# Optimization experiments

Hardware: AMD Instinct MI355X
Metric: run time of the kernel (lower is better)

## Reference

```python
import jax, jax.numpy as jnp
import numpy as np

B, N, F, T = 8, 4096, 3, 12
D = 64            # model_dim
AH, DK, DV = 4, 32, 32   # attention headers, k_dim, v_dim
GH = 8            # gat_headers == out_features
E = 524288


def _ln(x, g, b, eps=1e-5):
    m = jnp.mean(x, -1, keepdims=True)
    v = jnp.mean((x - m) ** 2, -1, keepdims=True)
    return (x - m) * jax.lax.rsqrt(v + eps) * g + b


def _glu(x, w, b, C):
    # x: [B, C, N, L], w: [2C, C, 1, k] -> causal-style valid conv + SiLU gate
    y = jax.lax.conv_general_dilated(x, w, (1, 1), 'VALID',
                                     dimension_numbers=('NCHW', 'OIHW', 'NCHW'))
    y = y + b[None, :, None, None]
    return jax.nn.silu(y[:, :C]) * y[:, C:]


def setup_inputs():
    key = jax.random.key(0)
    ks = jax.random.split(key, 20)
    s = jnp.float32(0.02)
    return {
        'data': jax.random.normal(ks[0], (B, N, F, T), jnp.float32),
        'edges': jax.random.randint(ks[1], (2, E), 0, B * N),
        'embT_w': jax.random.normal(ks[2], (T, N)) * s,
        'embT_g': jnp.ones((N,)), 'embT_b': jnp.zeros((N,)),
        'wq': jax.random.normal(ks[3], (N, AH * DK)) * s,
        'wk': jax.random.normal(ks[4], (N, AH * DK)) * s,
        'wv': jax.random.normal(ks[5], (N, AH * DV)) * s,
        'wo': jax.random.normal(ks[6], (AH * DV, N)) * s,
        'tat_g': jnp.ones((N,)), 'tat_b': jnp.zeros((N,)),
        'mix_w': jax.random.normal(ks[7], (D, T, F)) * s,
        'mix_b': jnp.zeros((D,)),
        'embS_w': jax.random.normal(ks[8], (N, D)) * s,
        'embS_g': jnp.ones((D,)), 'embS_b': jnp.zeros((D,)),
        'gat_wl': jax.random.normal(ks[9], (D, GH * T)) * s,
        'gat_bl': jnp.zeros((GH * T,)),
        'gat_wr': jax.random.normal(ks[10], (D, GH * T)) * s,
        'gat_br': jnp.zeros((GH * T,)),
        'gat_att': jax.random.normal(ks[11], (GH, T)) * s,
        'gat_bias': jnp.zeros((GH * T,)),
        'g3_w': jax.random.normal(ks[12], (2 * GH, GH, 1, 3)) * s, 'g3_b': jnp.zeros((2 * GH,)),
        'g5_w': jax.random.normal(ks[13], (2 * GH, GH, 1, 5)) * s, 'g5_b': jnp.zeros((2 * GH,)),
        'g7_w': jax.random.normal(ks[14], (2 * GH, GH, 1, 7)) * s, 'g7_b': jnp.zeros((2 * GH,)),
        'fc_w': jax.random.normal(ks[15], (3 * T - 12, T)) * s, 'fc_b': jnp.zeros((T,)),
        'res_w': jax.random.normal(ks[16], (GH, F)) * s, 'res_b': jnp.zeros((GH,)),
        'ln_g': jnp.ones((GH,)), 'ln_b': jnp.zeros((GH,)),
    }


def reference(data, edges, embT_w, embT_g, embT_b, wq, wk, wv, wo, tat_g, tat_b,
              mix_w, mix_b, embS_w, embS_g, embS_b,
              gat_wl, gat_bl, gat_wr, gat_br, gat_att, gat_bias,
              g3_w, g3_b, g5_w, g5_b, g7_w, g7_b, fc_w, fc_b,
              res_w, res_b, ln_g, ln_b):
    # ---- EmbedT: [B,N,F,T] -> [B,F,T,N] plus learned temporal positional table
    x = data.transpose(0, 2, 3, 1) + embT_w[None, None]
    x = _ln(x, embT_g, embT_b)

    # ---- Temporal MHA over T (model_dim = N), dropout = identity in eval
    resid = x
    q = (x @ wq).reshape(B, F, T, AH, DK)
    k = (x @ wk).reshape(B, F, T, AH, DK)
    v = (x @ wv).reshape(B, F, T, AH, DV)
    scores = jnp.einsum('bfqhd,bfkhd->bfhqk', q, k) / jnp.sqrt(jnp.float32(DK))
    attn = jax.nn.softmax(scores, axis=-1)
    ctx = jnp.einsum('bfhqk,bfkhd->bfqhd', attn, v).reshape(B, F, T, AH * DV)
    x = _ln(ctx @ wo + resid, tat_g, tat_b)

    # ---- feature_temporal_mixer: Conv2d(T, D, (1, F)) on [B,T,N,F] -> [B,N,D]
    x = jnp.einsum('bftn,dtf->bnd', x, mix_w) + mix_b

    # ---- EmbedS
    x = _ln(x + embS_w[None], embS_g, embS_b)

    # ---- GATv2Conv over B*N nodes (add_self_loops=True, leaky slope 0.2)
    BN = B * N
    xf = x.reshape(BN, D)
    xl = (xf @ gat_wl + gat_bl).reshape(BN, GH, T)
    xr = (xf @ gat_wr + gat_br).reshape(BN, GH, T)
    loop = jnp.arange(BN)
    src = jnp.concatenate([edges[0], loop])
    dst = jnp.concatenate([edges[1], loop])
    feat = jax.nn.leaky_relu(xl[src] + xr[dst], 0.2)          # [E+BN, GH, T]
    e = jnp.einsum('eht,ht->eh', feat, gat_att)
    m = jax.ops.segment_max(e, dst, num_segments=BN)
    ex = jnp.exp(e - m[dst])
    ssum = jax.ops.segment_sum(ex, dst, num_segments=BN)
    alpha = ex / ssum[dst]
    out = jax.ops.segment_sum(xl[src] * alpha[:, :, None], dst, num_segments=BN)
    out = out.reshape(BN, GH * T) + gat_bias

    res_gate = out.reshape(B, N, GH, T).transpose(0, 2, 1, 3)  # [B,GH,N,T]

    # ---- gated convs (GLU) kernels 3/5/7 -> concat -> fc
    g = jnp.concatenate([_glu(res_gate, g3_w, g3_b, GH),
                         _glu(res_gate, g5_w, g5_b, GH),
                         _glu(res_gate, g7_w, g7_b, GH)], axis=-1)  # [B,GH,N,3T-12]
    x = jax.nn.relu(g @ fc_w + fc_b)   # features_num == 3 branch

    # ---- residual 1x1 conv over feature channels of raw data
    x_res = jnp.einsum('bfnt,of->bont', data.transpose(0, 2, 1, 3), res_w) \
            + res_b[None, :, None, None]
    x = jax.nn.relu(x_res + x)         # [B,GH,N,T]
    x = _ln(x.transpose(0, 3, 2, 1), ln_g, ln_b)  # LN over GH on [B,T,N,GH]
    return x.transpose(0, 2, 3, 1)     # [B,N,GH,T]
```

## Files before the change

### kernel.cpp

```cpp
#include <hip/hip_runtime.h>
#include <hip/hip_bf16.h>

typedef __hip_bfloat16 bf16;
typedef short bf16x8 __attribute__((ext_vector_type(8)));
typedef float f32x4 __attribute__((ext_vector_type(4)));
typedef unsigned short u16x4 __attribute__((ext_vector_type(4)));

constexpr int B = 8, N = 4096, F = 3, T = 12;
constexpr int Dm = 64, AH = 4, DK = 32;
constexpr int GH = 8;
constexpr int E = 524288;
constexpr int BN = B * N;
constexpr int ROWS = B * F * T;
constexpr int HD = AH * DK;
constexpr int PSZ = ROWS * 384;

__device__ __forceinline__ float b2f(bf16 x) { return __bfloat162float(x); }
__device__ __forceinline__ float u2f(unsigned short u) {
  return __uint_as_float(((unsigned)u) << 16);
}

constexpr unsigned C_EMBTW=0, C_EMBTG=49152, C_EMBTB=53248, C_WQ=57344,
  C_WK=581632, C_WV=1105920, C_WO=1630208, C_TATG=2154496, C_TATB=2158592,
  C_MIXW=2162688, C_MIXB=2164992, C_EMBSW=2165056, C_EMBSG=2427200,
  C_EMBSB=2427264, C_GWL=2427328, C_GBL=2433472, C_GWR=2433568,
  C_GBR=2439712, C_GATT=2439808, C_GBIAS=2439904, C_G3W=2440000,
  C_G3B=2440384, C_G5W=2440400, C_G5B=2441040, C_G7W=2441056,
  C_G7B=2441952, C_FCW=2441968, C_FCB=2442256, C_RW=2442268, C_RB=2442292,
  C_LNG=2442300, C_LNB=2442308, C_TOT=2442316;

__device__ const unsigned CUM[33] = {
  0,49152,53248,57344,581632,1105920,1630208,2154496,2158592,2162688,
  2164992,2165056,2427200,2427264,2427328,2433472,2433568,2439712,2439808,
  2439904,2440000,2440384,2440400,2441040,2441056,2441952,2441968,2442256,
  2442268,2442292,2442300,2442308,2442316};

constexpr size_t OFF_CVT = 16;
constexpr size_t OFF_X1  = OFF_CVT + 2442320;
constexpr size_t OFF_CTXB= OFF_X1  + (size_t)ROWS * N;
constexpr size_t OFF_X2  = OFF_CTXB+ (size_t)ROWS * HD;
constexpr size_t OFF_X3  = OFF_X2  + (size_t)ROWS * N;
constexpr size_t OFF_XL  = OFF_X3  + (size_t)BN * Dm;
constexpr size_t OFF_XR  = OFF_XL  + (size_t)BN * GH * T / 2;
constexpr size_t OFF_RG  = OFF_XR  + (size_t)BN * GH * T / 2;
constexpr size_t OFF_INT = OFF_RG  + (size_t)BN * GH * T;
constexpr size_t OFF_X2R = OFF_INT + 600000;
constexpr size_t OFF_WT16 = OFF_RG;
constexpr size_t OFF_WO16 = OFF_RG + 786432;
constexpr size_t OFF_X1B  = OFF_RG + 786432 + 262144;
constexpr size_t OFF_PP   = OFF_X1B + 294912;
constexpr size_t OFF_WOT  = OFF_PP + 442368;
constexpr size_t OFF_GWT  = OFF_WOT + 262144;

struct Srcs { const void* p[32]; };
__global__ __launch_bounds__(256) void k_convert(
    const unsigned* __restrict__ g1, Srcs s, float* __restrict__ dst,
    bf16* __restrict__ wo16, int* __restrict__ cnt) {
  int f = (g1[0] != 0x3F800000u);
  for (unsigned gid = blockIdx.x * 256 + threadIdx.x;
       gid < C_TOT + 524288u + (unsigned)BN; gid += gridDim.x * 256) {
    if (gid < C_TOT) {
      int lo = 0, hi = 31;
      while (lo < hi) { int mid = (lo + hi + 1) >> 1; if (gid >= CUM[mid]) lo = mid; else hi = mid - 1; }
      if (lo >= 3 && lo <= 5) continue;
      unsigned off = gid - CUM[lo];
      dst[gid] = f ? b2f(((const bf16*)s.p[lo])[off]) : ((const float*)s.p[lo])[off];
    } else if (gid < C_TOT + 524288u) {
      unsigned off = gid - C_TOT;
      wo16[off] = f ? ((const bf16*)s.p[6])[off]
                    : __float2bfloat16(((const float*)s.p[6])[off]);
    } else {
      cnt[gid - C_TOT - 524288u] = 0;
    }
  }
}

__global__ __launch_bounds__(256) void k_wtrans(
    const unsigned* __restrict__ g1, const void* __restrict__ wq,
    const void* __restrict__ wk, const void* __restrict__ wv,
    bf16* __restrict__ wt) {
  __shared__ float t[32][33];
  int fl = (g1[0] != 0x3F800000u);
  int bid = blockIdx.x;
  int tc = bid / 128, tk = bid - tc * 128;
  int k0 = tk * 32, c0 = tc * 32;
  int mat = c0 >> 7, cloc = c0 & 127;
  const void* src = (mat == 0) ? wq : ((mat == 1) ? wk : wv);
  int tid = threadIdx.x;
  int r = tid >> 5, cc = tid & 31;
#pragma unroll
  for (int p = 0; p < 4; p++) {
    int row = p * 8 + r;
    size_t idx = (size_t)(k0 + row) * 128 + cloc + cc;
    t[row][cc] = fl ? b2f(((const bf16*)src)[idx]) : ((const float*)src)[idx];
  }
  __syncthreads();
#pragma unroll
  for (int p = 0; p < 4; p++) {
    int crow = p * 8 + r;
    wt[(size_t)(c0 + crow) * 4096 + k0 + cc] = __float2bfloat16(t[cc][crow]);
  }
}

__global__ __launch_bounds__(256) void k_wotrans(
    const bf16* __restrict__ wo, bf16* __restrict__ wot) {
  __shared__ bf16 t[32][33];
  int bid = blockIdx.x;
  int tn = bid >> 2, tk = bid & 3;
  int n0 = tn * 32, k0 = tk * 32;
  int tid = threadIdx.x;
  int r = tid >> 5, cc = tid & 31;
#pragma unroll
  for (int p = 0; p < 4; p++) {
    int row = p * 8 + r;
    t[row][cc] = wo[(size_t)(k0 + row) * 4096 + n0 + cc];
  }
  __syncthreads();
#pragma unroll
  for (int p = 0; p < 4; p++) {
    int crow = p * 8 + r;
    wot[(size_t)(n0 + crow) * 128 + k0 + cc] = t[cc][crow];
  }
}

__global__ __launch_bounds__(256) void k_gat_w(
    const float* __restrict__ wl, const float* __restrict__ wr,
    bf16* __restrict__ wlrt) {
  int idx = blockIdx.x * 256 + threadIdx.x;
  if (idx >= 192 * 64) return;
  int c = idx >> 6, k = idx & 63;
  float v = (c < 96) ? wl[(size_t)k * 96 + c] : wr[(size_t)k * 96 + (c - 96)];
  wlrt[idx] = __float2bfloat16(v);
}

__global__ __launch_bounds__(1024) void k_embt_ln(
    const unsigned* __restrict__ g1, const void* __restrict__ data,
    const float* __restrict__ w, const float* __restrict__ g,
    const float* __restrict__ b_, float* __restrict__ x1,
    bf16* __restrict__ x1b) {
  __shared__ float red[32];
  int row = blockIdx.x;
  int t = row % T; int bf_ = row / T; int f = bf_ % F; int bb = bf_ / F;
  int tid = threadIdx.x;
  int fl = (g1[0] != 0x3F800000u);
  float dv[4];
  if (fl) {
#pragma unroll
    for (int i = 0; i < 4; i++) {
      int n = i * 1024 + tid;
      dv[i] = b2f(((const bf16*)data)[(size_t)(bb * N + n) * 36 + f * 12 + t]);
    }
  } else {
#pragma unroll
    for (int i = 0; i < 4; i++) {
      int n = i * 1024 + tid;
      dv[i] = ((const float*)data)[(size_t)(bb * N + n) * 36 + f * 12 + t];
    }
  }
  float vals[4]; float s = 0.f, s2 = 0.f;
#pragma unroll
  for (int i = 0; i < 4; i++) {
    int n = i * 1024 + tid;
    float v = dv[i] + w[t * N + n];
    vals[i] = v; s += v; s2 += v * v;
  }
#pragma unroll
  for (int o = 32; o > 0; o >>= 1) { s += __shfl_down(s, o, 64); s2 += __shfl_down(s2, o, 64); }
  int lane = tid & 63, wid = tid >> 6;
  if (lane == 0) { red[wid] = s; red[16 + wid] = s2; }
  __syncthreads();
  float S = 0.f, S2 = 0.f;
#pragma unroll
  for (int j = 0; j < 16; j++) { S += red[j]; S2 += red[16 + j]; }
  float mean = S / (float)N;
  float var = S2 / (float)N - mean * mean;
  float inv = rsqrtf(var + 1e-5f);
#pragma unroll
  for (int i = 0; i < 4; i++) {
    int n = i * 1024 + tid;
    float o = (vals[i] - mean) * inv * g[n] + b_[n];
    x1[(size_t)row * N + n] = o;
    x1b[(size_t)row * N + n] = __float2bfloat16(o);
  }
}

__global__ __launch_bounds__(256) void k_qkv_mma(
    const bf16* __restrict__ x1b, const bf16* __restrict__ wt,
    float* __restrict__ pp) {
  int wave = (blockIdx.x * 256 + threadIdx.x) >> 6;
  int lane = threadIdx.x & 63;
  int ks = wave & 3, tile = wave >> 2;
  int mt = tile / 24, nt = tile - mt * 24;
  int m = lane & 15, quad = lane >> 4;
  const bf16* ap = x1b + (size_t)(mt * 16 + m) * 4096 + ks * 1024 + quad * 8;
  const bf16* bp = wt  + (size_t)(nt * 16 + m) * 4096 + ks * 1024 + quad * 8;
  f32x4 acc = {0.f, 0.f, 0.f, 0.f};
  for (int kk = 0; kk < 1024; kk += 32) {
    bf16x8 a = *(const bf16x8*)(ap + kk);
    bf16x8 b = *(const bf16x8*)(bp + kk);
    acc = __builtin_amdgcn_mfma_f32_16x16x32_bf16(a, b, acc, 0, 0, 0);
  }
  float* o = pp + ((size_t)ks * ROWS + mt * 16 + quad * 4) * 384 + nt * 16 + m;
#pragma unroll
  for (int r = 0; r < 4; r++) o[(size_t)r * 384] = acc[r];
}

__global__ __launch_bounds__(64) void k_attn(
    const float* __restrict__ pp, bf16* __restrict__ ctxb) {
  int blk = blockIdx.x; int h = blk & 3; int bf_ = blk >> 2;
  int tid = threadIdx.x;
  __shared__ float qs[12][32], ks[12][32], vs[12][32], att[12][12];
  for (int idx = tid; idx < 384; idx += 64) {
    int t = idx >> 5, d = idx & 31;
    int base = (bf_ * T + t) * 384 + h * 32 + d;
    qs[t][d] = pp[base] + pp[PSZ + base] + pp[2 * PSZ + base] + pp[3 * PSZ + base];
    ks[t][d] = pp[base + 128] + pp[PSZ + base + 128] + pp[2 * PSZ + base + 128] + pp[3 * PSZ + base + 128];
    vs[t][d] = pp[base + 256] + pp[PSZ + base + 256] + pp[2 * PSZ + base + 256] + pp[3 * PSZ + base + 256];
  }
  __syncthreads();
  for (int idx = tid; idx < 144; idx += 64) {
    int qt = idx / 12, kt = idx - qt * 12;
    float s = 0.f;
#pragma unroll
    for (int d = 0; d < 32; d++) s += qs[qt][d] * ks[kt][d];
    att[qt][kt] = s * 0.1767766953f;
  }
  __syncthreads();
  if (tid < 12) {
    float m = -1e30f;
#pragma unroll
    for (int j = 0; j < 12; j++) m = fmaxf(m, att[tid][j]);
    float ss = 0.f;
#pragma unroll
    for (int j = 0; j < 12; j++) { float e = __expf(att[tid][j] - m); att[tid][j] = e; ss += e; }
    float inv = 1.f / ss;
#pragma unroll
    for (int j = 0; j < 12; j++) att[tid][j] *= inv;
  }
  __syncthreads();
  for (int idx = tid; idx < 384; idx += 64) {
    int t = idx >> 5, d = idx & 31;
    float s = 0.f;
#pragma unroll
    for (int j = 0; j < 12; j++) s += att[t][j] * vs[j][d];
    ctxb[(size_t)(bf_ * T + t) * HD + h * 32 + d] = __float2bfloat16(s);
  }
}

__global__ __launch_bounds__(256) void k_proj_mma(
    const bf16* __restrict__ ctxb, const bf16* __restrict__ wot,
    const float* __restrict__ x1, float* __restrict__ x2r) {
  int wave = (blockIdx.x * 256 + threadIdx.x) >> 6;
  int lane = threadIdx.x & 63;
  int nt = wave & 255, mt = wave >> 8;
  int m = lane & 15, quad = lane >> 4;
  const bf16* ap = ctxb + (size_t)(mt * 16 + m) * 128 + quad * 8;
  const bf16* bp = wot  + (size_t)(nt * 16 + m) * 128 + quad * 8;
  f32x4 acc = {0.f, 0.f, 0.f, 0.f};
#pragma unroll
  for (int kk = 0; kk < 128; kk += 32) {
    bf16x8 a = *(const bf16x8*)(ap + kk);
    bf16x8 b = *(const bf16x8*)(bp + kk);
    acc = __builtin_amdgcn_mfma_f32_16x16x32_bf16(a, b, acc, 0, 0, 0);
  }
  int row0 = mt * 16 + quad * 4, col = nt * 16 + m;
#pragma unroll
  for (int r = 0; r < 4; r++) {
    size_t idx = (size_t)(row0 + r) * N + col;
    x2r[idx] = acc[r] + x1[idx];
  }
}

__global__ __launch_bounds__(1024) void k_ln2(
    const float* __restrict__ x2r, const float* __restrict__ g,
    const float* __restrict__ b_, float* __restrict__ x2) {
  __shared__ float red[32];
  int row = blockIdx.x, tid = threadIdx.x;
  float vals[4]; float s = 0.f, s2 = 0.f;
#pragma unroll
  for (int i = 0; i < 4; i++) {
    int n = i * 1024 + tid;
    float v = x2r[(size_t)row * N + n];
    vals[i] = v; s += v; s2 += v * v;
  }
#pragma unroll
  for (int o = 32; o > 0; o >>= 1) { s += __shfl_down(s, o, 64); s2 += __shfl_down(s2, o, 64); }
  int lane = tid & 63, wid = tid >> 6;
  if (lane == 0) { red[wid] = s; red[16 + wid] = s2; }
  __syncthreads();
  float S = 0.f, S2 = 0.f;
#pragma unroll
  for (int j = 0; j < 16; j++) { S += red[j]; S2 += red[16 + j]; }
  float mean = S / (float)N;
  float var = S2 / (float)N - mean * mean;
  float inv = rsqrtf(var + 1e-5f);
#pragma unroll
  for (int i = 0; i < 4; i++) {
    int n = i * 1024 + tid;
    x2[(size_t)row * N + n] = (vals[i] - mean) * inv * g[n] + b_[n];
  }
}

__global__ __launch_bounds__(256) void k_mix_ln(
    const float* __restrict__ x2, const float* __restrict__ mw,
    const float* __restrict__ mb, const float* __restrict__ sw,
    const float* __restrict__ g, const float* __restrict__ b_,
    bf16* __restrict__ x3b) {
  int tid = threadIdx.x; int wid = tid >> 6; int d = tid & 63;
  int ng = blockIdx.x * 4 + wid;
  int bb = ng >> 12; int n = ng & (N - 1);
  float acc = mb[d];
#pragma unroll
  for (int t = 0; t < T; t++)
#pragma unroll
    for (int f = 0; f < F; f++)
      acc += x2[((size_t)(bb * F + f) * T + t) * N + n] * mw[(d * T + t) * F + f];
  acc += sw[(size_t)n * Dm + d];
  float s = acc, s2 = acc * acc;
#pragma unroll
  for (int m = 1; m < 64; m <<= 1) { s += __shfl_xor(s, m, 64); s2 += __shfl_xor(s2, m, 64); }
  float mean = s * (1.f / 64.f), var = s2 * (1.f / 64.f) - mean * mean;
  float inv = rsqrtf(var + 1e-5f);
  x3b[(size_t)ng * Dm + d] = __float2bfloat16((acc - mean) * inv * g[d] + b_[d]);
}

__global__ __launch_bounds__(256) void k_gat_mma(
    const bf16* __restrict__ x3b, const bf16* __restrict__ wlrt,
    const float* __restrict__ bl, const float* __restrict__ br,
    bf16* __restrict__ xl, bf16* __restrict__ xr) {
  __shared__ __align__(16) bf16 bs[192 * 64];
  int tid = threadIdx.x;
  {
    const bf16x8* src = (const bf16x8*)wlrt;
    bf16x8* dst = (bf16x8*)bs;
#pragma unroll
    for (int i = 0; i < 6; i++) {
      int ci = i * 256 + tid;
      dst[ci ^ ((ci >> 3) & 7)] = src[ci];
    }
  }
  __syncthreads();
  int wave = tid >> 6, lane = tid & 63;
  int mt = blockIdx.x * 4 + wave;
  int m = lane & 15, quad = lane >> 4;
  const bf16* ap = x3b + (size_t)(mt * 16 + m) * 64 + quad * 8;
  bf16x8 a0 = *(const bf16x8*)(ap);
  bf16x8 a1 = *(const bf16x8*)(ap + 32);
  const bf16x8* bs8 = (const bf16x8*)bs;
  int row0 = mt * 16 + quad * 4;
#pragma unroll
  for (int nt = 0; nt < 12; nt++) {
    int r = nt * 16 + m;
    int c0 = r * 8 + quad;
    bf16x8 b0 = bs8[c0 ^ (r & 7)];
    bf16x8 b1 = bs8[(c0 + 4) ^ (r & 7)];
    f32x4 acc = {0.f, 0.f, 0.f, 0.f};
    acc = __builtin_amdgcn_mfma_f32_16x16x32_bf16(a0, b0, acc, 0, 0, 0);
    acc = __builtin_amdgcn_mfma_f32_16x16x32_bf16(a1, b1, acc, 0, 0, 0);
    bool left = r < 96;
    int c = left ? r : r - 96;
    float bias = left ? bl[c] : br[c];
    bf16* o = left ? xl : xr;
#pragma unroll
    for (int rr = 0; rr < 4; rr++)
      o[(size_t)(row0 + rr) * 96 + c] = __float2bfloat16(acc[rr] + bias);
  }
}

__global__ __launch_bounds__(256) void k_hist(
    const int* __restrict__ edges, int* __restrict__ cnt) {
  int e = blockIdx.x * 256 + threadIdx.x;
  if (e < E) atomicAdd(cnt + edges[E + e], 1);
}

__global__ __launch_bounds__(1024) void k_scan(
    const int* __restrict__ cnt, int* __restrict__ off, int* __restrict__ cur) {
  __shared__ int part[1024];
  int tid = threadIdx.x;
  int base = tid * 32;
  int local[32]; int s = 0;
#pragma unroll
  for (int j = 0; j < 32; j++) { local[j] = cnt[base + j]; s += local[j]; }
  part[tid] = s;
  __syncthreads();
  for (int d = 1; d < 1024; d <<= 1) {
    int v = (tid >= d) ? part[tid - d] : 0;
    __syncthreads();
    part[tid] += v;
    __syncthreads();
  }
  int run = part[tid] - s;
#pragma unroll
  for (int j = 0; j < 32; j++) {
    off[base + j] = run; cur[base + j] = run;
    run += local[j];
  }
  if (tid == 1023) off[BN] = E;
}

__global__ __launch_bounds__(256) void k_scatter(
    const int* __restrict__ edges, int* __restrict__ cur, int* __restrict__ srcs) {
  int e = blockIdx.x * 256 + threadIdx.x;
  if (e < E) {
    int pos = atomicAdd(cur + edges[E + e], 1);
    srcs[pos] = edges[e];
  }
}

__device__ __forceinline__ void ld12bf(const bf16* p, float* l) {
  u16x4 a = *(const u16x4*)p;
  u16x4 b = *(const u16x4*)(p + 4);
  u16x4 c = *(const u16x4*)(p + 8);
  l[0]=u2f(a.x); l[1]=u2f(a.y); l[2]=u2f(a.z); l[3]=u2f(a.w);
  l[4]=u2f(b.x); l[5]=u2f(b.y); l[6]=u2f(b.z); l[7]=u2f(b.w);
  l[8]=u2f(c.x); l[9]=u2f(c.y); l[10]=u2f(c.z); l[11]=u2f(c.w);
}

__global__ __launch_bounds__(256) void k_gat(
    const int* __restrict__ off, const int* __restrict__ srcs,
    const bf16* __restrict__ xl, const bf16* __restrict__ xr,
    const float* __restrict__ att, const float* __restrict__ bias,
    float* __restrict__ rg) {
  int tid = threadIdx.x;
  int g = tid >> 3, h = tid & 7;
  int dst = blockIdx.x * 32 + g;
  int bb = dst >> 12, n = dst & (N - 1);
  size_t rbase = (size_t)dst * 96 + h * 12;
  float xd[12], at[12];
  ld12bf(xr + rbase, xd);
#pragma unroll
  for (int t = 0; t < 12; t++) at[t] = att[h * 12 + t];

  float acc[12]; float ssum;
  {
    float l[12];
    ld12bf(xl + rbase, l);
    float sc = 0.f;
#pragma unroll
    for (int t = 0; t < 12; t++) {
      float sv = l[t] + xd[t];
      float fr = sv > 0.f ? sv : 0.2f * sv;
      sc += fr * at[t];
    }
    float ex = __expf(sc);
    ssum = ex;
#pragma unroll
    for (int t = 0; t < 12; t++) acc[t] = l[t] * ex;
  }
  int st = off[dst], en = off[dst + 1];
  for (int j = st; j < en; j++) {
    int src = srcs[j];
    float l[12];
    ld12bf(xl + (size_t)src * 96 + h * 12, l);
    float sc = 0.f;
#pragma unroll
    for (int t = 0; t < 12; t++) {
      float sv = l[t] + xd[t];
      float fr = sv > 0.f ? sv : 0.2f * sv;
      sc += fr * at[t];
    }
    float ex = __expf(sc);
    ssum += ex;
#pragma unroll
    for (int t = 0; t < 12; t++) acc[t] += l[t] * ex;
  }
  float inv = 1.f / ssum;
  float* op = rg + ((size_t)(bb * 8 + h) * N + n) * 12;
#pragma unroll
  for (int t = 0; t < 12; t++)
    op[t] = acc[t] * inv + bias[h * 12 + t];
}

__global__ __launch_bounds__(768) void k_tail(
    const unsigned* __restrict__ g1, const float* __restrict__ rg,
    const float* __restrict__ g3w, const float* __restrict__ g3b,
    const float* __restrict__ g5w, const float* __restrict__ g5b,
    const float* __restrict__ g7w, const float* __restrict__ g7b,
    const float* __restrict__ fcw, const float* __restrict__ fcb,
    const void* __restrict__ data, const float* __restrict__ rw,
    const float* __restrict__ rb, const float* __restrict__ lng,
    const float* __restrict__ lnb, void* __restrict__ out) {
  int tid = threadIdx.x;
  int br = tid >> 8;
  int u = tid & 255;
  int h = u & 7, i = u >> 3;
  int blk = blockIdx.x;
  int bb = blk >> 7;
  int n0 = (blk & 127) * 32;
  int n = n0 + i;
  int fl = (g1[0] != 0x3F800000u);
  __shared__ float xs[32][100];
  __shared__ float dds[32][40];
  __shared__ float wpk[8 * 260 + 4];
  __shared__ float fcs[288];
  __shared__ float gbuf[24][256];
  __shared__ float b3s[16], b5s[16], b7s[16], fcbs[12], lngs[8], lnbs[8], rws[24], rbs[8];
  for (int idx = tid; idx < 3072; idx += 768) {
    int c = idx / 384; int within = idx - c * 384;
    int ii = within / 12, t = within - ii * 12;
    xs[ii][c * 12 + t] = rg[((size_t)(bb * 8 + c) * N + n0 + ii) * 12 + t];
  }
  if (fl) {
    for (int idx = tid; idx < 1152; idx += 768) {
      int nn = idx / 36, jj = idx - nn * 36;
      dds[nn][jj] = b2f(((const bf16*)data)[(size_t)(bb * N + n0 + nn) * 36 + jj]);
    }
  } else {
    for (int idx = tid; idx < 1152; idx += 768) {
      int nn = idx / 36, jj = idx - nn * 36;
      dds[nn][jj] = ((const float*)data)[(size_t)(bb * N + n0 + nn) * 36 + jj];
    }
  }
  for (int idx = tid; idx < 1920; idx += 768) {
    int hh = idx / 240; int r = idx - hh * 240; int c = r / 30; int tap = r - c * 30;
    float v;
    if (tap < 3)       v = g3w[hh * 24 + c * 3 + tap];
    else if (tap < 6)  v = g3w[(hh + 8) * 24 + c * 3 + (tap - 3)];
    else if (tap < 11) v = g5w[hh * 40 + c * 5 + (tap - 6)];
    else if (tap < 16) v = g5w[(hh + 8) * 40 + c * 5 + (tap - 11)];
    else if (tap < 23) v = g7w[hh * 56 + c * 7 + (tap - 16)];
    else               v = g7w[(hh + 8) * 56 + c * 7 + (tap - 23)];
    wpk[hh * 260 + c * 32 + tap] = v;
  }
  for (int idx = tid; idx < 288; idx += 768) fcs[idx] = fcw[idx];
  if (tid < 16) { b3s[tid] = g3b[tid]; b5s[tid] = g5b[tid]; b7s[tid] = g7b[tid]; }
  if (tid < 12) fcbs[tid] = fcb[tid];
  if (tid < 24) rws[tid] = rw[tid];
  if (tid < 8) { lngs[tid] = lng[tid]; lnbs[tid] = lnb[tid]; rbs[tid] = rb[tid]; }
  __syncthreads();
  const float* x = xs[i];
  const float* wbase = &wpk[h * 260];
  if (br == 0) {
    float pa[10], pb[10];
    float ba = b3s[h], bbv = b3s[h + 8];
#pragma unroll
    for (int l = 0; l < 10; l++) { pa[l] = ba; pb[l] = bbv; }
#pragma unroll
    for (int c = 0; c < 8; c++) {
      float4 xa = *(const float4*)&x[c * 12];
      float4 xb = *(const float4*)&x[c * 12 + 4];
      float4 xc = *(const float4*)&x[c * 12 + 8];
      float xr[12] = {xa.x, xa.y, xa.z, xa.w, xb.x, xb.y, xb.z, xb.w,
                      xc.x, xc.y, xc.z, xc.w};
      const float* wpc = wbase + c * 32;
      float4 wA = *(const float4*)wpc;
      float2 wB = *(const float2*)(wpc + 4);
#pragma unroll
      for (int l = 0; l < 10; l++) {
        pa[l] += xr[l] * wA.x + xr[l + 1] * wA.y + xr[l + 2] * wA.z;
        pb[l] += xr[l] * wA.w + xr[l + 1] * wB.x + xr[l + 2] * wB.y;
      }
    }
#pragma unroll
    for (int l = 0; l < 10; l++)
      gbuf[l][u] = pa[l] / (1.f + __expf(-pa[l])) * pb[l];
  } else if (br == 1) {
    float pa[8], pb[8];
    float ba = b5s[h], bbv = b5s[h + 8];
#pragma unroll
    for (int l = 0; l < 8; l++) { pa[l] = ba; pb[l] = bbv; }
#pragma unroll
    for (int c = 0; c < 8; c++) {
      float4 xa = *(const float4*)&x[c * 12];
      float4 xb = *(const float4*)&x[c * 12 + 4];
      float4 xc = *(const float4*)&x[c * 12 + 8];
      float xr[12] = {xa.x, xa.y, xa.z, xa.w, xb.x, xb.y, xb.z, xb.w,
                      xc.x, xc.y, xc.z, xc.w};
      const float* wpc = wbase + c * 32;
      float2 w0 = *(const float2*)(wpc + 6);
      float2 w1 = *(const float2*)(wpc + 8);
      float2 w2 = *(const float2*)(wpc + 10);
      float2 w3 = *(const float2*)(wpc + 12);
      float2 w4 = *(const float2*)(wpc + 14);
      float wt[10] = {w0.x, w0.y, w1.x, w1.y, w2.x, w2.y, w3.x, w3.y, w4.x, w4.y};
#pragma unroll
      for (int l = 0; l < 8; l++) {
        float a = 0.f, bsum = 0.f;
#pragma unroll
        for (int j = 0; j < 5; j++) { a += xr[l + j] * wt[j]; bsum += xr[l + j] * wt[5 + j]; }
        pa[l] += a; pb[l] += bsum;
      }
    }
#pragma unroll
    for (int l = 0; l < 8; l++)
      gbuf[10 + l][u] = pa[l] / (1.f + __expf(-pa[l])) * pb[l];
  } else {
    float pa[6], pb[6];
    float ba = b7s[h], bbv = b7s[h + 8];
#pragma unroll
    for (int l = 0; l < 6; l++) { pa[l] = ba; pb[l] = bbv; }
#pragma unroll
    for (int c = 0; c < 8; c++) {
      float4 xa = *(const float4*)&x[c * 12];
      float4 xb = *(const float4*)&x[c * 12 + 4];
      float4 xc = *(const float4*)&x[c * 12 + 8];
      float xr[12] = {xa.x, xa.y, xa.z, xa.w, xb.x, xb.y, xb.z, xb.w,
                      xc.x, xc.y, xc.z, xc.w};
      const float* wpc = wbase + c * 32;
      float4 wA = *(const float4*)(wpc + 16);
      float4 wB = *(const float4*)(wpc + 20);
      float4 wC = *(const float4*)(wpc + 24);
      float2 wD = *(const float2*)(wpc + 28);
      float wt[14] = {wA.x, wA.y, wA.z, wA.w, wB.x, wB.y, wB.z, wB.w,
                      wC.x, wC.y, wC.z, wC.w, wD.x, wD.y};
#pragma unroll
      for (int l = 0; l < 6; l++) {
        float a = 0.f, bsum = 0.f;
#pragma unroll
        for (int j = 0; j < 7; j++) { a += xr[l + j] * wt[j]; bsum += xr[l + j] * wt[7 + j]; }
        pa[l] += a; pb[l] += bsum;
      }
    }
#pragma unroll
    for (int l = 0; l < 6; l++)
      gbuf[18 + l][u] = pa[l] / (1.f + __expf(-pa[l])) * pb[l];
  }
  __syncthreads();
  if (br == 0) {
    float gv[24];
#pragma unroll
    for (int l = 0; l < 24; l++) gv[l] = gbuf[l][u];
    float rw0 = rws[h * 3 + 0], rw1 = rws[h * 3 + 1], rw2 = rws[h * 3 + 2], rb0 = rbs[h];
    size_t obase = ((size_t)(bb * N + n) * GH + h) * T;
#pragma unroll
    for (int t = 0; t < 12; t++) {
      float a = fcbs[t];
#pragma unroll
      for (int l = 0; l < 24; l++) a += gv[l] * fcs[l * 12 + t];
      a = fmaxf(a, 0.f);
      float r = rb0 + dds[i][t] * rw0 + dds[i][12 + t] * rw1 + dds[i][24 + t] * rw2;
      float v = fmaxf(a + r, 0.f);
      float s = v, s2 = v * v;
#pragma unroll
      for (int m = 1; m < 8; m <<= 1) { s += __shfl_xor(s, m, 64); s2 += __shfl_xor(s2, m, 64); }
      float mean = s * 0.125f, var = s2 * 0.125f - mean * mean;
      float inv = rsqrtf(var + 1e-5f);
      float o = (v - mean) * inv * lngs[h] + lnbs[h];
      if (fl) ((bf16*)out)[obase + t] = __float2bfloat16(o);
      else    ((float*)out)[obase + t] = o;
    }
  }
}

extern "C" void kernel_launch(void* const* d_in, const int* in_sizes, int n_in,
                              void* d_out, int out_size, void* d_ws, size_t ws_size,
                              hipStream_t stream) {
  const void* data  = d_in[0];
  const int*  edges = (const int*)d_in[1];
  const unsigned* g1 = (const unsigned*)d_in[3];

  float* ws = (float*)d_ws;
  float* cv  = ws + OFF_CVT;
  float* x1  = ws + OFF_X1;  float* x2 = ws + OFF_X2;
  float* x2r = ws + OFF_X2R;
  bf16* x3b  = (bf16*)(ws + OFF_X3);
  bf16* ctxb = (bf16*)(ws + OFF_CTXB);
  bf16* xl   = (bf16*)(ws + OFF_XL);
  bf16* xr   = (bf16*)(ws + OFF_XR);
  float* rg  = ws + OFF_RG;
  bf16* wt16 = (bf16*)(ws + OFF_WT16);
  bf16* wo16 = (bf16*)(ws + OFF_WO16);
  bf16* x1b  = (bf16*)(ws + OFF_X1B);
  bf16* wot16= (bf16*)(ws + OFF_WOT);
  bf16* wlrt = (bf16*)(ws + OFF_GWT);
  float* pp  = ws + OFF_PP;
  int* ibase = (int*)(ws + OFF_INT);
  int* cnt  = ibase;
  int* off  = ibase + BN;
  int* srcs = ibase + 2 * BN + 16;

  Srcs s;
  for (int i = 0; i < 32; i++) s.p[i] = d_in[2 + i];

  k_convert<<<2048, 256, 0, stream>>>(g1, s, cv, wo16, cnt);
  k_wtrans<<<12 * 128, 256, 0, stream>>>(g1, d_in[5], d_in[6], d_in[7], wt16);
  k_wotrans<<<512, 256, 0, stream>>>(wo16, wot16);
  k_gat_w<<<48, 256, 0, stream>>>(cv + C_GWL, cv + C_GWR, wlrt);
  k_embt_ln<<<ROWS, 1024, 0, stream>>>(g1, data, cv + C_EMBTW, cv + C_EMBTG,
                                       cv + C_EMBTB, x1, x1b);
  k_qkv_mma<<<432, 256, 0, stream>>>(x1b, wt16, pp);
  k_attn<<<B * F * AH, 64, 0, stream>>>(pp, ctxb);
  k_proj_mma<<<1152, 256, 0, stream>>>(ctxb, wot16, x1, x2r);
  k_ln2<<<ROWS, 1024, 0, stream>>>(x2r, cv + C_TATG, cv + C_TATB, x2);
  k_mix_ln<<<BN / 4, 256, 0, stream>>>(x2, cv + C_MIXW, cv + C_MIXB, cv + C_EMBSW,
                                       cv + C_EMBSG, cv + C_EMBSB, x3b);
  k_gat_mma<<<512, 256, 0, stream>>>(x3b, wlrt, cv + C_GBL, cv + C_GBR, xl, xr);
  k_hist<<<E / 256, 256, 0, stream>>>(edges, cnt);
  k_scan<<<1, 1024, 0, stream>>>(cnt, off, cnt);
  k_scatter<<<E / 256, 256, 0, stream>>>(edges, cnt, srcs);
  k_gat<<<BN / 32, 256, 0, stream>>>(off, srcs, xl, xr, cv + C_GATT, cv + C_GBIAS, rg);
  k_tail<<<BN / 32, 768, 0, stream>>>(g1, rg, cv + C_G3W, cv + C_G3B, cv + C_G5W,
                                      cv + C_G5B, cv + C_G7W, cv + C_G7B, cv + C_FCW,
                                      cv + C_FCB, data, cv + C_RW, cv + C_RB,
                                      cv + C_LNG, cv + C_LNB, d_out);
}
```

Baseline: 352.3 us.

## Split GAT edge loop across lanes and double QKV split-K

The GAT aggregation kernel now gives one wave per destination node. Eight lane groups each take a strided slice of that node's incoming edges, and the partial softmax sums and weighted accumulators are combined with xor-shuffle reductions. The QKV MFMA split-K factor goes from 4 to 8, doubling the number of waves, and the attention kernel sums eight partial buffers instead of four. The aim is more parallelism and latency hiding on the irregular edge loop and the small GEMM. In exchange it adds shuffle reduction overhead, more partial-sum traffic and a larger workspace region, and lanes sit idle when a node has fewer than eight edges (about 16 on average).

```diff
diff --git a/kernel.cpp b/kernel.cpp
--- a/kernel.cpp
+++ b/kernel.cpp
@@ -14,6 +14,7 @@
 constexpr int ROWS = B * F * T;
 constexpr int HD = AH * DK;
 constexpr int PSZ = ROWS * 384;
+constexpr int KSPLIT = 8;
 
 __device__ __forceinline__ float b2f(bf16 x) { return __bfloat162float(x); }
 __device__ __forceinline__ float u2f(unsigned short u) {
@@ -49,7 +50,7 @@
 constexpr size_t OFF_WO16 = OFF_RG + 786432;
 constexpr size_t OFF_X1B  = OFF_RG + 786432 + 262144;
 constexpr size_t OFF_PP   = OFF_X1B + 294912;
-constexpr size_t OFF_WOT  = OFF_PP + 442368;
+constexpr size_t OFF_WOT  = OFF_PP + (size_t)KSPLIT * PSZ;
 constexpr size_t OFF_GWT  = OFF_WOT + 262144;
 
 struct Srcs { const void* p[32]; };
@@ -189,13 +190,13 @@
     float* __restrict__ pp) {
   int wave = (blockIdx.x * 256 + threadIdx.x) >> 6;
   int lane = threadIdx.x & 63;
-  int ks = wave & 3, tile = wave >> 2;
+  int ks = wave & 7, tile = wave >> 3;
   int mt = tile / 24, nt = tile - mt * 24;
   int m = lane & 15, quad = lane >> 4;
-  const bf16* ap = x1b + (size_t)(mt * 16 + m) * 4096 + ks * 1024 + quad * 8;
-  const bf16* bp = wt  + (size_t)(nt * 16 + m) * 4096 + ks * 1024 + quad * 8;
+  const bf16* ap = x1b + (size_t)(mt * 16 + m) * 4096 + ks * 512 + quad * 8;
+  const bf16* bp = wt  + (size_t)(nt * 16 + m) * 4096 + ks * 512 + quad * 8;
   f32x4 acc = {0.f, 0.f, 0.f, 0.f};
-  for (int kk = 0; kk < 1024; kk += 32) {
+  for (int kk = 0; kk < 512; kk += 32) {
     bf16x8 a = *(const bf16x8*)(ap + kk);
     bf16x8 b = *(const bf16x8*)(bp + kk);
     acc = __builtin_amdgcn_mfma_f32_16x16x32_bf16(a, b, acc, 0, 0, 0);
@@ -213,9 +214,14 @@
   for (int idx = tid; idx < 384; idx += 64) {
     int t = idx >> 5, d = idx & 31;
     int base = (bf_ * T + t) * 384 + h * 32 + d;
-    qs[t][d] = pp[base] + pp[PSZ + base] + pp[2 * PSZ + base] + pp[3 * PSZ + base];
-    ks[t][d] = pp[base + 128] + pp[PSZ + base + 128] + pp[2 * PSZ + base + 128] + pp[3 * PSZ + base + 128];
-    vs[t][d] = pp[base + 256] + pp[PSZ + base + 256] + pp[2 * PSZ + base + 256] + pp[3 * PSZ + base + 256];
+    float qv = 0.f, kv = 0.f, vv = 0.f;
+#pragma unroll
+    for (int p = 0; p < KSPLIT; p++) {
+      qv += pp[(size_t)p * PSZ + base];
+      kv += pp[(size_t)p * PSZ + base + 128];
+      vv += pp[(size_t)p * PSZ + base + 256];
+    }
+    qs[t][d] = qv; ks[t][d] = kv; vs[t][d] = vv;
   }
   __syncthreads();
   for (int idx = tid; idx < 144; idx += 64) {
@@ -422,8 +428,9 @@
     const float* __restrict__ att, const float* __restrict__ bias,
     float* __restrict__ rg) {
   int tid = threadIdx.x;
-  int g = tid >> 3, h = tid & 7;
-  int dst = blockIdx.x * 32 + g;
+  int wv = tid >> 6, lane = tid & 63;
+  int es = lane >> 3, h = lane & 7;
+  int dst = blockIdx.x * 4 + wv;
   int bb = dst >> 12, n = dst & (N - 1);
   size_t rbase = (size_t)dst * 96 + h * 12;
   float xd[12], at[12];
@@ -431,8 +438,11 @@
 #pragma unroll
   for (int t = 0; t < 12; t++) at[t] = att[h * 12 + t];
 
-  float acc[12]; float ssum;
-  {
+  float acc[12];
+#pragma unroll
+  for (int t = 0; t < 12; t++) acc[t] = 0.f;
+  float ssum = 0.f;
+  if (es == 0) {
     float l[12];
     ld12bf(xl + rbase, l);
     float sc = 0.f;
@@ -448,7 +458,7 @@
     for (int t = 0; t < 12; t++) acc[t] = l[t] * ex;
   }
   int st = off[dst], en = off[dst + 1];
-  for (int j = st; j < en; j++) {
+  for (int j = st + es; j < en; j += 8) {
     int src = srcs[j];
     float l[12];
     ld12bf(xl + (size_t)src * 96 + h * 12, l);
@@ -464,11 +474,19 @@
 #pragma unroll
     for (int t = 0; t < 12; t++) acc[t] += l[t] * ex;
   }
-  float inv = 1.f / ssum;
-  float* op = rg + ((size_t)(bb * 8 + h) * N + n) * 12;
-#pragma unroll
-  for (int t = 0; t < 12; t++)
-    op[t] = acc[t] * inv + bias[h * 12 + t];
+#pragma unroll
+  for (int m = 8; m < 64; m <<= 1) {
+    ssum += __shfl_xor(ssum, m, 64);
+#pragma unroll
+    for (int t = 0; t < 12; t++) acc[t] += __shfl_xor(acc[t], m, 64);
+  }
+  if (es == 0) {
+    float inv = 1.f / ssum;
+    float* op = rg + ((size_t)(bb * 8 + h) * N + n) * 12;
+#pragma unroll
+    for (int t = 0; t < 12; t++)
+      op[t] = acc[t] * inv + bias[h * 12 + t];
+  }
 }
 
 __global__ __launch_bounds__(768) void k_tail(
@@ -678,7 +696,7 @@
   k_gat_w<<<48, 256, 0, stream>>>(cv + C_GWL, cv + C_GWR, wlrt);
   k_embt_ln<<<ROWS, 1024, 0, stream>>>(g1, data, cv + C_EMBTW, cv + C_EMBTG,
                                        cv + C_EMBTB, x1, x1b);
-  k_qkv_mma<<<432, 256, 0, stream>>>(x1b, wt16, pp);
+  k_qkv_mma<<<864, 256, 0, stream>>>(x1b, wt16, pp);
   k_attn<<<B * F * AH, 64, 0, stream>>>(pp, ctxb);
   k_proj_mma<<<1152, 256, 0, stream>>>(ctxb, wot16, x1, x2r);
   k_ln2<<<ROWS, 1024, 0, stream>>>(x2r, cv + C_TATG, cv + C_TATB, x2);
@@ -688,7 +706,7 @@
   k_hist<<<E / 256, 256, 0, stream>>>(edges, cnt);
   k_scan<<<1, 1024, 0, stream>>>(cnt, off, cnt);
   k_scatter<<<E / 256, 256, 0, stream>>>(edges, cnt, srcs);
-  k_gat<<<BN / 32, 256, 0, stream>>>(off, srcs, xl, xr, cv + C_GATT, cv + C_GBIAS, rg);
+  k_gat<<<BN / 4, 256, 0, stream>>>(off, srcs, xl, xr, cv + C_GATT, cv + C_GBIAS, rg);
   k_tail<<<BN / 32, 768, 0, stream>>>(g1, rg, cv + C_G3W, cv + C_G3B, cv + C_G5W,
                                       cv + C_G5B, cv + C_G7W, cv + C_G7B, cv + C_FCW,
                                       cv + C_FCB, data, cv + C_RW, cv + C_RB,
```

After: 352.3 us. No clear change (-0.0%).
